# Optimization experiments

Measured on AMD Instinct MI355X. Metric: run time of the kernel, lower is better.

## Reference

```python
import jax, jax.numpy as jnp
import numpy as np

FIELD_DIMS = [100000, 50000, 1000, 500, 100, 50, 20, 10]
INPUT_DIM = sum(FIELD_DIMS)            # 151680
NUM_FIELDS = len(FIELD_DIMS)           # 8
FACTOR_DIM = 16
HIDDEN = [256, 128]
OFFSETS = np.concatenate([[0], np.cumsum(FIELD_DIMS)[:-1]]).astype(np.int32)
BATCH = 2048
EPS = 1e-5


def setup_inputs() -> dict:
    key = jax.random.key(0)
    ks = jax.random.split(key, 32)
    # per-field indices, each within its own cardinality
    x = jnp.stack([
        jax.random.randint(ks[f], (BATCH,), 0, FIELD_DIMS[f], dtype=jnp.int32)
        for f in range(NUM_FIELDS)
    ], axis=1)  # [B, F]
    # concatenated embedding tables (xavier_uniform per torch init, approximated with uniform)
    lim = float(np.sqrt(6.0 / (max(FIELD_DIMS) + FACTOR_DIM)))
    emb_table = jax.random.uniform(ks[8], (INPUT_DIM, FACTOR_DIM), minval=-lim, maxval=lim, dtype=jnp.float32)
    # FM linear: weight ~ N(0, 0.01), bias 0
    w_lin = 0.01 * jax.random.normal(ks[9], (INPUT_DIM,), dtype=jnp.float32)
    b_lin = jnp.zeros((), dtype=jnp.float32)
    d0 = NUM_FIELDS * FACTOR_DIM  # 128
    def lin(k, fan_in, fan_out):
        b = float(np.sqrt(1.0 / fan_in))
        kw, kb = jax.random.split(k)
        W = jax.random.uniform(kw, (fan_in, fan_out), minval=-b, maxval=b, dtype=jnp.float32)
        bias = jax.random.uniform(kb, (fan_out,), minval=-b, maxval=b, dtype=jnp.float32)
        return W, bias
    W1, b1 = lin(ks[10], d0, HIDDEN[0])
    W2, b2 = lin(ks[11], HIDDEN[0], HIDDEN[1])
    W3, b3 = lin(ks[12], HIDDEN[1], 1)
    g1 = jnp.ones((HIDDEN[0],), jnp.float32); be1 = jnp.zeros((HIDDEN[0],), jnp.float32)
    g2 = jnp.ones((HIDDEN[1],), jnp.float32); be2 = jnp.zeros((HIDDEN[1],), jnp.float32)
    return {"x": x, "emb_table": emb_table, "w_lin": w_lin, "b_lin": b_lin,
            "W1": W1, "b1": b1, "g1": g1, "be1": be1,
            "W2": W2, "b2": b2, "g2": g2, "be2": be2,
            "W3": W3, "b3": b3}


def _batchnorm(h, gamma, beta):
    # training-mode BN (torch default): biased batch variance
    m = jnp.mean(h, axis=0)
    v = jnp.mean((h - m) ** 2, axis=0)
    return gamma * (h - m) / jnp.sqrt(v + EPS) + beta


def reference(x, emb_table, w_lin, b_lin, W1, b1, g1, be1, W2, b2, g2, be2, W3, b3):
    B = x.shape[0]
    offsets = jnp.asarray(OFFSETS)
    # --- faithful to original bug: scatter one-hot uses RAW x (no field offsets) ---
    sparse_x = jnp.zeros((B, INPUT_DIM), jnp.float32).at[
        jnp.arange(B)[:, None], x].set(1.0)  # duplicates collapse to 1.0, like scatter_
    y_linear = sparse_x @ w_lin + b_lin  # [B]
    # --- dense field embeddings (offset gather into concatenated table) ---
    dense_x = emb_table[x + offsets[None, :]]  # [B, F, K]
    s = jnp.sum(dense_x, axis=1)               # [B, K]
    square_of_sum = s * s
    sum_of_square = jnp.sum(dense_x * dense_x, axis=1)
    y_pairwise = 0.5 * jnp.sum(square_of_sum - sum_of_square, axis=1)  # [B]
    y_fm = y_linear + y_pairwise
    # --- DNN on concatenated embeddings ---
    h = dense_x.reshape(B, NUM_FIELDS * FACTOR_DIM)
    h = jax.nn.relu(_batchnorm(h @ W1 + b1, g1, be1))
    h = jax.nn.relu(_batchnorm(h @ W2 + b2, g2, be2))
    y_dnn = (h @ W3 + b3)[:, 0]  # [B]
    return y_fm + y_dnn
```

## Files before the change

kernel.cpp:

```cpp
#include <hip/hip_runtime.h>

#define EPS 1e-5f

static __device__ const int OFFS[8] = {0, 100000, 150000, 151000, 151500, 151600, 151650, 151670};

__global__ __launch_bounds__(256) void k1_gather_fm_gemm1(
    const int* __restrict__ x, const float* __restrict__ emb,
    const float* __restrict__ wlin, const float* __restrict__ blin,
    const float* __restrict__ W1, const float* __restrict__ b1,
    float* __restrict__ yfm, float* __restrict__ z1, float* __restrict__ p1)
{
    __shared__ float h0s[16][128];
    const int t = threadIdx.x;
    const int blk = blockIdx.x;
    const int r = t >> 4, l = t & 15;
    const int b = blk * 16 + r;

    int idx[8];
#pragma unroll
    for (int f = 0; f < 8; ++f) idx[f] = x[b * 8 + f];

    float s = 0.f, ssq = 0.f;
#pragma unroll
    for (int f = 0; f < 8; ++f) {
        float e = emb[(idx[f] + OFFS[f]) * 16 + l];
        h0s[r][f * 16 + l] = e;
        s += e;
        ssq += e * e;
    }
    float pair = s * s - ssq;
#pragma unroll
    for (int m = 8; m >= 1; m >>= 1) pair += __shfl_xor(pair, m);

    if (l == 0) {
        float lin = 0.f;
#pragma unroll
        for (int f = 0; f < 8; ++f) {
            bool dup = false;
            for (int g = 0; g < f; ++g) dup = dup || (idx[g] == idx[f]);
            if (!dup) lin += wlin[idx[f]];
        }
        yfm[b] = 0.5f * pair + lin + blin[0];
    }
    __syncthreads();

    const int j = t;
    float acc[16];
#pragma unroll
    for (int r2 = 0; r2 < 16; ++r2) acc[r2] = 0.f;
    for (int k = 0; k < 128; ++k) {
        float w = W1[k * 256 + j];
#pragma unroll
        for (int r2 = 0; r2 < 16; ++r2) acc[r2] += h0s[r2][k] * w;
    }
    const float bj = b1[j];
    float zsum = 0.f, zss = 0.f;
#pragma unroll
    for (int r2 = 0; r2 < 16; ++r2) {
        float z = acc[r2] + bj;
        z1[(blk * 16 + r2) * 256 + j] = z;
        zsum += z;
        zss += z * z;
    }
    p1[blk * 512 + j] = zsum;
    p1[blk * 512 + 256 + j] = zss;
}

__global__ __launch_bounds__(256) void k2_bn1_gemm2(
    const float* __restrict__ z1, const float* __restrict__ p1,
    const float* __restrict__ g1, const float* __restrict__ be1,
    const float* __restrict__ W2, const float* __restrict__ b2,
    float* __restrict__ z2, float* __restrict__ p2)
{
    __shared__ float h1s[32][256];
    __shared__ float psum[2][128];
    __shared__ float pss[2][128];
    const int t = threadIdx.x, blk = blockIdx.x;

    float sum = 0.f, ss = 0.f;
    for (int q = 0; q < 128; ++q) {
        sum += p1[q * 512 + t];
        ss  += p1[q * 512 + 256 + t];
    }
    const float mean = sum * (1.f / 2048.f);
    const float var  = ss * (1.f / 2048.f) - mean * mean;
    const float scale = g1[t] / sqrtf(var + EPS);
    const float shift = be1[t] - mean * scale;

    for (int r = 0; r < 32; ++r) {
        float z = z1[(blk * 32 + r) * 256 + t];
        float h = z * scale + shift;
        h1s[r][t] = h > 0.f ? h : 0.f;
    }
    __syncthreads();

    const int j = t & 127, half = t >> 7;
    float acc[16];
#pragma unroll
    for (int r = 0; r < 16; ++r) acc[r] = 0.f;
    for (int k = 0; k < 256; ++k) {
        float w = W2[k * 128 + j];
#pragma unroll
        for (int r = 0; r < 16; ++r) acc[r] += h1s[half * 16 + r][k] * w;
    }
    const float bj = b2[j];
    float zsum = 0.f, zss = 0.f;
#pragma unroll
    for (int r = 0; r < 16; ++r) {
        float z = acc[r] + bj;
        z2[(blk * 32 + half * 16 + r) * 128 + j] = z;
        zsum += z;
        zss += z * z;
    }
    psum[half][j] = zsum;
    pss[half][j] = zss;
    __syncthreads();
    if (half == 0) {
        p2[blk * 256 + j]       = psum[0][j] + psum[1][j];
        p2[blk * 256 + 128 + j] = pss[0][j] + pss[1][j];
    }
}

__global__ __launch_bounds__(256) void k3_bn2_out(
    const float* __restrict__ z2, const float* __restrict__ p2,
    const float* __restrict__ g2, const float* __restrict__ be2,
    const float* __restrict__ W3, const float* __restrict__ b3,
    const float* __restrict__ yfm, float* __restrict__ out)
{
    __shared__ float scl[128], shf[128];
    const int t = threadIdx.x, blk = blockIdx.x;
    if (t < 128) {
        float sum = 0.f, ss = 0.f;
        for (int q = 0; q < 64; ++q) {
            sum += p2[q * 256 + t];
            ss  += p2[q * 256 + 128 + t];
        }
        const float mean = sum * (1.f / 2048.f);
        const float var  = ss * (1.f / 2048.f) - mean * mean;
        const float sc = g2[t] / sqrtf(var + EPS);
        scl[t] = sc;
        shf[t] = be2[t] - mean * sc;
    }
    __syncthreads();

    const int r = t >> 3, l8 = t & 7;
    const int b = blk * 32 + r;
    float acc = 0.f;
#pragma unroll
    for (int q = 0; q < 16; ++q) {
        int k = q * 8 + l8;
        float z = z2[b * 128 + k];
        float h = z * scl[k] + shf[k];
        h = h > 0.f ? h : 0.f;
        acc += h * W3[k];
    }
#pragma unroll
    for (int m = 4; m >= 1; m >>= 1) acc += __shfl_xor(acc, m);
    if (l8 == 0) out[b] = acc + b3[0] + yfm[b];
}

extern "C" void kernel_launch(void* const* d_in, const int* in_sizes, int n_in,
                              void* d_out, int out_size, void* d_ws, size_t ws_size,
                              hipStream_t stream) {
    const int*   x    = (const int*)d_in[0];
    const float* emb  = (const float*)d_in[1];
    const float* wlin = (const float*)d_in[2];
    const float* blin = (const float*)d_in[3];
    const float* W1   = (const float*)d_in[4];
    const float* b1   = (const float*)d_in[5];
    const float* g1   = (const float*)d_in[6];
    const float* be1  = (const float*)d_in[7];
    const float* W2   = (const float*)d_in[8];
    const float* b2   = (const float*)d_in[9];
    const float* g2   = (const float*)d_in[10];
    const float* be2  = (const float*)d_in[11];
    const float* W3   = (const float*)d_in[12];
    const float* b3   = (const float*)d_in[13];

    float* ws  = (float*)d_ws;
    float* yfm = ws;
    float* z1  = yfm + 2048;
    float* p1  = z1 + 2048 * 256;
    float* z2  = p1 + 128 * 512;
    float* p2  = z2 + 2048 * 128;
    float* out = (float*)d_out;

    k1_gather_fm_gemm1<<<128, 256, 0, stream>>>(x, emb, wlin, blin, W1, b1, yfm, z1, p1);
    k2_bn1_gemm2<<<64, 256, 0, stream>>>(z1, p1, g1, be1, W2, b2, z2, p2);
    k3_bn2_out<<<64, 256, 0, stream>>>(z2, p2, g2, be2, W3, b3, yfm, out);
}
```

Measured before the change: 44.79 us.

## Repartition all three kernels across more blocks with vectorized loads and split reductions

```diff
diff --git a/kernel.cpp b/kernel.cpp
--- a/kernel.cpp
+++ b/kernel.cpp
@@ -10,114 +10,161 @@
     const float* __restrict__ W1, const float* __restrict__ b1,
     float* __restrict__ yfm, float* __restrict__ z1, float* __restrict__ p1)
 {
-    __shared__ float h0s[16][128];
+    __shared__ __align__(16) float h0s[16][128];
+    __shared__ __align__(16) float red[2][8][128];
     const int t = threadIdx.x;
-    const int blk = blockIdx.x;
-    const int r = t >> 4, l = t & 15;
-    const int b = blk * 16 + r;
-
-    int idx[8];
-#pragma unroll
-    for (int f = 0; f < 8; ++f) idx[f] = x[b * 8 + f];
-
-    float s = 0.f, ssq = 0.f;
-#pragma unroll
-    for (int f = 0; f < 8; ++f) {
-        float e = emb[(idx[f] + OFFS[f]) * 16 + l];
-        h0s[r][f * 16 + l] = e;
-        s += e;
-        ssq += e * e;
-    }
-    float pair = s * s - ssq;
-#pragma unroll
-    for (int m = 8; m >= 1; m >>= 1) pair += __shfl_xor(pair, m);
-
-    if (l == 0) {
-        float lin = 0.f;
+    const int rt = blockIdx.x >> 1;
+    const int ch = blockIdx.x & 1;
+
+    {
+        const int g_r = t >> 4, g_l = t & 15;
+        const int b = rt * 16 + g_r;
+        int idx[8];
+#pragma unroll
+        for (int f = 0; f < 8; ++f) idx[f] = x[b * 8 + f];
+
+        float s = 0.f, ssq = 0.f;
 #pragma unroll
         for (int f = 0; f < 8; ++f) {
-            bool dup = false;
-            for (int g = 0; g < f; ++g) dup = dup || (idx[g] == idx[f]);
-            if (!dup) lin += wlin[idx[f]];
-        }
-        yfm[b] = 0.5f * pair + lin + blin[0];
-    }
-    __syncthreads();
-
-    const int j = t;
-    float acc[16];
-#pragma unroll
-    for (int r2 = 0; r2 < 16; ++r2) acc[r2] = 0.f;
-    for (int k = 0; k < 128; ++k) {
-        float w = W1[k * 256 + j];
-#pragma unroll
-        for (int r2 = 0; r2 < 16; ++r2) acc[r2] += h0s[r2][k] * w;
-    }
-    const float bj = b1[j];
-    float zsum = 0.f, zss = 0.f;
-#pragma unroll
-    for (int r2 = 0; r2 < 16; ++r2) {
-        float z = acc[r2] + bj;
-        z1[(blk * 16 + r2) * 256 + j] = z;
-        zsum += z;
-        zss += z * z;
-    }
-    p1[blk * 512 + j] = zsum;
-    p1[blk * 512 + 256 + j] = zss;
-}
-
-__global__ __launch_bounds__(256) void k2_bn1_gemm2(
+            float e = emb[(idx[f] + OFFS[f]) * 16 + g_l];
+            h0s[g_r][f * 16 + g_l] = e;
+            s += e;
+            ssq += e * e;
+        }
+        if (ch == 0) {
+            float pair = s * s - ssq;
+#pragma unroll
+            for (int m = 8; m >= 1; m >>= 1) pair += __shfl_xor(pair, m);
+            if (g_l == 0) {
+                float lin = 0.f;
+#pragma unroll
+                for (int f = 0; f < 8; ++f) {
+                    bool dup = false;
+                    for (int g = 0; g < f; ++g) dup = dup || (idx[g] == idx[f]);
+                    if (!dup) lin += wlin[idx[f]];
+                }
+                yfm[b] = 0.5f * pair + lin + blin[0];
+            }
+        }
+    }
+    __syncthreads();
+
+    const int jg = t & 31, rp = t >> 5;
+    const float* Wb = W1 + ch * 128 + jg * 4;
+    float acc0[4] = {0.f, 0.f, 0.f, 0.f};
+    float acc1[4] = {0.f, 0.f, 0.f, 0.f};
+    for (int k = 0; k < 128; k += 4) {
+        float4 ha = *(const float4*)&h0s[rp * 2][k];
+        float4 hb = *(const float4*)&h0s[rp * 2 + 1][k];
+        const float ha_[4] = {ha.x, ha.y, ha.z, ha.w};
+        const float hb_[4] = {hb.x, hb.y, hb.z, hb.w};
+#pragma unroll
+        for (int kk = 0; kk < 4; ++kk) {
+            float4 w = *(const float4*)&Wb[(k + kk) * 256];
+            acc0[0] += ha_[kk] * w.x; acc0[1] += ha_[kk] * w.y;
+            acc0[2] += ha_[kk] * w.z; acc0[3] += ha_[kk] * w.w;
+            acc1[0] += hb_[kk] * w.x; acc1[1] += hb_[kk] * w.y;
+            acc1[2] += hb_[kk] * w.z; acc1[3] += hb_[kk] * w.w;
+        }
+    }
+    float4 bj = *(const float4*)&b1[ch * 128 + jg * 4];
+    const float bj_[4] = {bj.x, bj.y, bj.z, bj.w};
+    float zs[4], zss[4];
+    float z0[4], z1v[4];
+#pragma unroll
+    for (int c = 0; c < 4; ++c) {
+        z0[c] = acc0[c] + bj_[c];
+        z1v[c] = acc1[c] + bj_[c];
+        zs[c] = z0[c] + z1v[c];
+        zss[c] = z0[c] * z0[c] + z1v[c] * z1v[c];
+    }
+    const int r0 = rt * 16 + rp * 2;
+    *(float4*)&z1[r0 * 256 + ch * 128 + jg * 4] = make_float4(z0[0], z0[1], z0[2], z0[3]);
+    *(float4*)&z1[(r0 + 1) * 256 + ch * 128 + jg * 4] = make_float4(z1v[0], z1v[1], z1v[2], z1v[3]);
+    *(float4*)&red[0][rp][jg * 4] = make_float4(zs[0], zs[1], zs[2], zs[3]);
+    *(float4*)&red[1][rp][jg * 4] = make_float4(zss[0], zss[1], zss[2], zss[3]);
+    __syncthreads();
+    if (t < 128) {
+        float s = 0.f, ss = 0.f;
+#pragma unroll
+        for (int q = 0; q < 8; ++q) { s += red[0][q][t]; ss += red[1][q][t]; }
+        p1[rt * 512 + ch * 128 + t] = s;
+        p1[rt * 512 + 256 + ch * 128 + t] = ss;
+    }
+}
+
+__global__ __launch_bounds__(512) void k2_bn1_gemm2(
     const float* __restrict__ z1, const float* __restrict__ p1,
     const float* __restrict__ g1, const float* __restrict__ be1,
     const float* __restrict__ W2, const float* __restrict__ b2,
     float* __restrict__ z2, float* __restrict__ p2)
 {
-    __shared__ float h1s[32][256];
-    __shared__ float psum[2][128];
-    __shared__ float pss[2][128];
-    const int t = threadIdx.x, blk = blockIdx.x;
-
-    float sum = 0.f, ss = 0.f;
-    for (int q = 0; q < 128; ++q) {
-        sum += p1[q * 512 + t];
-        ss  += p1[q * 512 + 256 + t];
-    }
-    const float mean = sum * (1.f / 2048.f);
-    const float var  = ss * (1.f / 2048.f) - mean * mean;
-    const float scale = g1[t] / sqrtf(var + EPS);
-    const float shift = be1[t] - mean * scale;
-
-    for (int r = 0; r < 32; ++r) {
-        float z = z1[(blk * 32 + r) * 256 + t];
-        float h = z * scale + shift;
-        h1s[r][t] = h > 0.f ? h : 0.f;
-    }
-    __syncthreads();
-
-    const int j = t & 127, half = t >> 7;
-    float acc[16];
-#pragma unroll
-    for (int r = 0; r < 16; ++r) acc[r] = 0.f;
-    for (int k = 0; k < 256; ++k) {
-        float w = W2[k * 128 + j];
-#pragma unroll
-        for (int r = 0; r < 16; ++r) acc[r] += h1s[half * 16 + r][k] * w;
-    }
-    const float bj = b2[j];
-    float zsum = 0.f, zss = 0.f;
-#pragma unroll
-    for (int r = 0; r < 16; ++r) {
-        float z = acc[r] + bj;
-        z2[(blk * 32 + half * 16 + r) * 128 + j] = z;
-        zsum += z;
-        zss += z * z;
-    }
-    psum[half][j] = zsum;
-    pss[half][j] = zss;
-    __syncthreads();
-    if (half == 0) {
-        p2[blk * 256 + j]       = psum[0][j] + psum[1][j];
-        p2[blk * 256 + 128 + j] = pss[0][j] + pss[1][j];
+    __shared__ __align__(16) float h1s[8][256];
+    __shared__ __align__(16) float sclS[256], shfS[256];
+    __shared__ __align__(16) float sp[2][256], ssp[2][256];
+    __shared__ __align__(16) float red2[2][8][128];
+    const int t = threadIdx.x, rb = blockIdx.x;
+
+    {
+        const int col = t & 255, h = t >> 8;
+        float s = 0.f, ss = 0.f;
+#pragma unroll 16
+        for (int q = h * 64; q < h * 64 + 64; ++q) {
+            s += p1[q * 512 + col];
+            ss += p1[q * 512 + 256 + col];
+        }
+        sp[h][col] = s; ssp[h][col] = ss;
+    }
+    __syncthreads();
+    if (t < 256) {
+        float s = sp[0][t] + sp[1][t];
+        float ss = ssp[0][t] + ssp[1][t];
+        float mean = s * (1.f / 2048.f);
+        float var = ss * (1.f / 2048.f) - mean * mean;
+        float sc = g1[t] * __frsqrt_rn(var + EPS);
+        sclS[t] = sc;
+        shfS[t] = be1[t] - mean * sc;
+    }
+    __syncthreads();
+
+    {
+        const int lr = t >> 6, lc = (t & 63) * 4;
+        float4 zv = *(const float4*)&z1[(rb * 8 + lr) * 256 + lc];
+        float4 sc = *(const float4*)&sclS[lc];
+        float4 sh = *(const float4*)&shfS[lc];
+        float4 hv;
+        hv.x = fmaxf(zv.x * sc.x + sh.x, 0.f);
+        hv.y = fmaxf(zv.y * sc.y + sh.y, 0.f);
+        hv.z = fmaxf(zv.z * sc.z + sh.z, 0.f);
+        hv.w = fmaxf(zv.w * sc.w + sh.w, 0.f);
+        *(float4*)&h1s[lr][lc] = hv;
+    }
+    __syncthreads();
+
+    const int r = t >> 6, j2 = (t & 63) * 2;
+    float acc[2] = {0.f, 0.f};
+    for (int k = 0; k < 256; k += 4) {
+        float4 hv = *(const float4*)&h1s[r][k];
+        const float h_[4] = {hv.x, hv.y, hv.z, hv.w};
+#pragma unroll
+        for (int kk = 0; kk < 4; ++kk) {
+            float2 w = *(const float2*)&W2[(k + kk) * 128 + j2];
+            acc[0] += h_[kk] * w.x;
+            acc[1] += h_[kk] * w.y;
+        }
+    }
+    float2 bj = *(const float2*)&b2[j2];
+    float za = acc[0] + bj.x, zb = acc[1] + bj.y;
+    *(float2*)&z2[(rb * 8 + r) * 128 + j2] = make_float2(za, zb);
+    *(float2*)&red2[0][r][j2] = make_float2(za, zb);
+    *(float2*)&red2[1][r][j2] = make_float2(za * za, zb * zb);
+    __syncthreads();
+    if (t < 128) {
+        float s = 0.f, ss = 0.f;
+#pragma unroll
+        for (int q = 0; q < 8; ++q) { s += red2[0][q][t]; ss += red2[1][q][t]; }
+        p2[rb * 256 + t] = s;
+        p2[rb * 256 + 128 + t] = ss;
     }
 }
 
@@ -127,36 +174,44 @@
     const float* __restrict__ W3, const float* __restrict__ b3,
     const float* __restrict__ yfm, float* __restrict__ out)
 {
-    __shared__ float scl[128], shf[128];
+    __shared__ __align__(16) float sp[2][128], ssp[2][128];
+    __shared__ __align__(16) float scl[128], shf[128];
     const int t = threadIdx.x, blk = blockIdx.x;
+    {
+        const int col = t & 127, h = t >> 7;
+        float s = 0.f, ss = 0.f;
+#pragma unroll 16
+        for (int q = h * 128; q < h * 128 + 128; ++q) {
+            s += p2[q * 256 + col];
+            ss += p2[q * 256 + 128 + col];
+        }
+        sp[h][col] = s; ssp[h][col] = ss;
+    }
+    __syncthreads();
     if (t < 128) {
-        float sum = 0.f, ss = 0.f;
-        for (int q = 0; q < 64; ++q) {
-            sum += p2[q * 256 + t];
-            ss  += p2[q * 256 + 128 + t];
-        }
-        const float mean = sum * (1.f / 2048.f);
-        const float var  = ss * (1.f / 2048.f) - mean * mean;
-        const float sc = g2[t] / sqrtf(var + EPS);
+        float s = sp[0][t] + sp[1][t];
+        float ss = ssp[0][t] + ssp[1][t];
+        float mean = s * (1.f / 2048.f);
+        float var = ss * (1.f / 2048.f) - mean * mean;
+        float sc = g2[t] * __frsqrt_rn(var + EPS);
         scl[t] = sc;
         shf[t] = be2[t] - mean * sc;
     }
     __syncthreads();
 
-    const int r = t >> 3, l8 = t & 7;
-    const int b = blk * 32 + r;
-    float acc = 0.f;
-#pragma unroll
-    for (int q = 0; q < 16; ++q) {
-        int k = q * 8 + l8;
-        float z = z2[b * 128 + k];
-        float h = z * scl[k] + shf[k];
-        h = h > 0.f ? h : 0.f;
-        acc += h * W3[k];
-    }
-#pragma unroll
-    for (int m = 4; m >= 1; m >>= 1) acc += __shfl_xor(acc, m);
-    if (l8 == 0) out[b] = acc + b3[0] + yfm[b];
+    const int r = t >> 5, l32 = t & 31;
+    const int b = blk * 8 + r;
+    float4 zv = *(const float4*)&z2[b * 128 + l32 * 4];
+    float4 sc = *(const float4*)&scl[l32 * 4];
+    float4 sh = *(const float4*)&shf[l32 * 4];
+    float4 wv = *(const float4*)&W3[l32 * 4];
+    float acc = fmaxf(zv.x * sc.x + sh.x, 0.f) * wv.x
+              + fmaxf(zv.y * sc.y + sh.y, 0.f) * wv.y
+              + fmaxf(zv.z * sc.z + sh.z, 0.f) * wv.z
+              + fmaxf(zv.w * sc.w + sh.w, 0.f) * wv.w;
+#pragma unroll
+    for (int m = 16; m >= 1; m >>= 1) acc += __shfl_xor(acc, m);
+    if (l32 == 0) out[b] = acc + b3[0] + yfm[b];
 }
 
 extern "C" void kernel_launch(void* const* d_in, const int* in_sizes, int n_in,
@@ -185,7 +240,7 @@
     float* p2  = z2 + 2048 * 128;
     float* out = (float*)d_out;
 
-    k1_gather_fm_gemm1<<<128, 256, 0, stream>>>(x, emb, wlin, blin, W1, b1, yfm, z1, p1);
-    k2_bn1_gemm2<<<64, 256, 0, stream>>>(z1, p1, g1, be1, W2, b2, z2, p2);
-    k3_bn2_out<<<64, 256, 0, stream>>>(z2, p2, g2, be2, W3, b3, yfm, out);
-}
+    k1_gather_fm_gemm1<<<256, 256, 0, stream>>>(x, emb, wlin, blin, W1, b1, yfm, z1, p1);
+    k2_bn1_gemm2<<<256, 512, 0, stream>>>(z1, p1, g1, be1, W2, b2, z2, p2);
+    k3_bn2_out<<<256, 256, 0, stream>>>(z2, p2, g2, be2, W3, b3, yfm, out);
+}
```

Result: faster. 37.84 us (-15.5%).

## Fuse three DeepFM kernels into one cooperative kernel with grid syncs

Applied to the files above, without the earlier changes.

```diff
diff --git a/kernel.cpp b/kernel.cpp
--- a/kernel.cpp
+++ b/kernel.cpp
@@ -1,162 +1,236 @@
 #include <hip/hip_runtime.h>
+#include <hip/hip_cooperative_groups.h>
+
+namespace cg = cooperative_groups;
 
 #define EPS 1e-5f
 
 static __device__ const int OFFS[8] = {0, 100000, 150000, 151000, 151500, 151600, 151650, 151670};
 
-__global__ __launch_bounds__(256) void k1_gather_fm_gemm1(
+__global__ __launch_bounds__(256) void deepfm_fused(
     const int* __restrict__ x, const float* __restrict__ emb,
     const float* __restrict__ wlin, const float* __restrict__ blin,
     const float* __restrict__ W1, const float* __restrict__ b1,
-    float* __restrict__ yfm, float* __restrict__ z1, float* __restrict__ p1)
-{
-    __shared__ float h0s[16][128];
-    const int t = threadIdx.x;
-    const int blk = blockIdx.x;
-    const int r = t >> 4, l = t & 15;
-    const int b = blk * 16 + r;
-
-    int idx[8];
-#pragma unroll
-    for (int f = 0; f < 8; ++f) idx[f] = x[b * 8 + f];
-
-    float s = 0.f, ssq = 0.f;
-#pragma unroll
-    for (int f = 0; f < 8; ++f) {
-        float e = emb[(idx[f] + OFFS[f]) * 16 + l];
-        h0s[r][f * 16 + l] = e;
-        s += e;
-        ssq += e * e;
-    }
-    float pair = s * s - ssq;
-#pragma unroll
-    for (int m = 8; m >= 1; m >>= 1) pair += __shfl_xor(pair, m);
-
-    if (l == 0) {
-        float lin = 0.f;
-#pragma unroll
-        for (int f = 0; f < 8; ++f) {
-            bool dup = false;
-            for (int g = 0; g < f; ++g) dup = dup || (idx[g] == idx[f]);
-            if (!dup) lin += wlin[idx[f]];
-        }
-        yfm[b] = 0.5f * pair + lin + blin[0];
-    }
-    __syncthreads();
-
-    const int j = t;
-    float acc[16];
-#pragma unroll
-    for (int r2 = 0; r2 < 16; ++r2) acc[r2] = 0.f;
-    for (int k = 0; k < 128; ++k) {
-        float w = W1[k * 256 + j];
-#pragma unroll
-        for (int r2 = 0; r2 < 16; ++r2) acc[r2] += h0s[r2][k] * w;
-    }
-    const float bj = b1[j];
-    float zsum = 0.f, zss = 0.f;
-#pragma unroll
-    for (int r2 = 0; r2 < 16; ++r2) {
-        float z = acc[r2] + bj;
-        z1[(blk * 16 + r2) * 256 + j] = z;
-        zsum += z;
-        zss += z * z;
-    }
-    p1[blk * 512 + j] = zsum;
-    p1[blk * 512 + 256 + j] = zss;
-}
-
-__global__ __launch_bounds__(256) void k2_bn1_gemm2(
-    const float* __restrict__ z1, const float* __restrict__ p1,
     const float* __restrict__ g1, const float* __restrict__ be1,
     const float* __restrict__ W2, const float* __restrict__ b2,
-    float* __restrict__ z2, float* __restrict__ p2)
-{
-    __shared__ float h1s[32][256];
-    __shared__ float psum[2][128];
-    __shared__ float pss[2][128];
-    const int t = threadIdx.x, blk = blockIdx.x;
-
-    float sum = 0.f, ss = 0.f;
-    for (int q = 0; q < 128; ++q) {
-        sum += p1[q * 512 + t];
-        ss  += p1[q * 512 + 256 + t];
-    }
-    const float mean = sum * (1.f / 2048.f);
-    const float var  = ss * (1.f / 2048.f) - mean * mean;
-    const float scale = g1[t] / sqrtf(var + EPS);
-    const float shift = be1[t] - mean * scale;
-
-    for (int r = 0; r < 32; ++r) {
-        float z = z1[(blk * 32 + r) * 256 + t];
-        float h = z * scale + shift;
-        h1s[r][t] = h > 0.f ? h : 0.f;
-    }
-    __syncthreads();
-
-    const int j = t & 127, half = t >> 7;
-    float acc[16];
-#pragma unroll
-    for (int r = 0; r < 16; ++r) acc[r] = 0.f;
-    for (int k = 0; k < 256; ++k) {
-        float w = W2[k * 128 + j];
-#pragma unroll
-        for (int r = 0; r < 16; ++r) acc[r] += h1s[half * 16 + r][k] * w;
-    }
-    const float bj = b2[j];
-    float zsum = 0.f, zss = 0.f;
-#pragma unroll
-    for (int r = 0; r < 16; ++r) {
-        float z = acc[r] + bj;
-        z2[(blk * 32 + half * 16 + r) * 128 + j] = z;
-        zsum += z;
-        zss += z * z;
-    }
-    psum[half][j] = zsum;
-    pss[half][j] = zss;
-    __syncthreads();
-    if (half == 0) {
-        p2[blk * 256 + j]       = psum[0][j] + psum[1][j];
-        p2[blk * 256 + 128 + j] = pss[0][j] + pss[1][j];
-    }
-}
-
-__global__ __launch_bounds__(256) void k3_bn2_out(
-    const float* __restrict__ z2, const float* __restrict__ p2,
     const float* __restrict__ g2, const float* __restrict__ be2,
     const float* __restrict__ W3, const float* __restrict__ b3,
-    const float* __restrict__ yfm, float* __restrict__ out)
+    float* __restrict__ p1g, float* __restrict__ s1g,
+    float* __restrict__ p2g, float* __restrict__ s2g,
+    float* __restrict__ out)
 {
-    __shared__ float scl[128], shf[128];
+    cg::grid_group grid = cg::this_grid();
+
+    __shared__ __align__(16) float h0s[8][128];
+    __shared__ __align__(16) float h1s[8][256];
+    __shared__ __align__(16) float redA[8][256];
+    __shared__ __align__(16) float redB[8][256];
+    __shared__ __align__(16) float wsS[4][4], wsQ[4][4];
+    __shared__ float yfmS[8];
+
     const int t = threadIdx.x, blk = blockIdx.x;
+    const int rp = t >> 5, l = t & 31;
+    const int row = blk * 8 + rp;
+
+    {
+        const int f = l >> 2, dq = (l & 3) * 4;
+        const int idxf = x[row * 8 + f];
+        float4 e = *(const float4*)&emb[(size_t)(idxf + OFFS[f]) * 16 + dq];
+        *(float4*)&h0s[rp][f * 16 + dq] = e;
+
+        float4 s = e;
+        float4 q = make_float4(e.x * e.x, e.y * e.y, e.z * e.z, e.w * e.w);
+#pragma unroll
+        for (int m = 4; m <= 16; m <<= 1) {
+            s.x += __shfl_xor(s.x, m); s.y += __shfl_xor(s.y, m);
+            s.z += __shfl_xor(s.z, m); s.w += __shfl_xor(s.w, m);
+            q.x += __shfl_xor(q.x, m); q.y += __shfl_xor(q.y, m);
+            q.z += __shfl_xor(q.z, m); q.w += __shfl_xor(q.w, m);
+        }
+        float pair = (s.x * s.x - q.x) + (s.y * s.y - q.y)
+                   + (s.z * s.z - q.z) + (s.w * s.w - q.w);
+        pair += __shfl_xor(pair, 1);
+        pair += __shfl_xor(pair, 2);
+
+        float lin = 0.f;
+        if (l < 8) {
+            int ids[8];
+#pragma unroll
+            for (int f2 = 0; f2 < 8; ++f2) ids[f2] = x[row * 8 + f2];
+            bool dup = false;
+            for (int g = 0; g < l; ++g) dup = dup || (ids[g] == ids[l]);
+            lin = dup ? 0.f : wlin[ids[l]];
+        }
+        lin += __shfl_xor(lin, 1);
+        lin += __shfl_xor(lin, 2);
+        lin += __shfl_xor(lin, 4);
+        if (l == 0) yfmS[rp] = 0.5f * pair + lin + blin[0];
+    }
+    __syncthreads();
+
+    float z1r[8];
+    {
+        float acc[8] = {0.f, 0.f, 0.f, 0.f, 0.f, 0.f, 0.f, 0.f};
+        const float* Wb = W1 + l * 8;
+        for (int k = 0; k < 128; k += 4) {
+            float4 h4 = *(const float4*)&h0s[rp][k];
+            const float h_[4] = {h4.x, h4.y, h4.z, h4.w};
+#pragma unroll
+            for (int kk = 0; kk < 4; ++kk) {
+                float4 wA = *(const float4*)&Wb[(k + kk) * 256];
+                float4 wB = *(const float4*)&Wb[(k + kk) * 256 + 4];
+                acc[0] += h_[kk] * wA.x; acc[1] += h_[kk] * wA.y;
+                acc[2] += h_[kk] * wA.z; acc[3] += h_[kk] * wA.w;
+                acc[4] += h_[kk] * wB.x; acc[5] += h_[kk] * wB.y;
+                acc[6] += h_[kk] * wB.z; acc[7] += h_[kk] * wB.w;
+            }
+        }
+        float4 bA = *(const float4*)&b1[l * 8];
+        float4 bB = *(const float4*)&b1[l * 8 + 4];
+        z1r[0] = acc[0] + bA.x; z1r[1] = acc[1] + bA.y;
+        z1r[2] = acc[2] + bA.z; z1r[3] = acc[3] + bA.w;
+        z1r[4] = acc[4] + bB.x; z1r[5] = acc[5] + bB.y;
+        z1r[6] = acc[6] + bB.z; z1r[7] = acc[7] + bB.w;
+
+        *(float4*)&redA[rp][l * 8]     = make_float4(z1r[0], z1r[1], z1r[2], z1r[3]);
+        *(float4*)&redA[rp][l * 8 + 4] = make_float4(z1r[4], z1r[5], z1r[6], z1r[7]);
+        *(float4*)&redB[rp][l * 8]     = make_float4(z1r[0]*z1r[0], z1r[1]*z1r[1], z1r[2]*z1r[2], z1r[3]*z1r[3]);
+        *(float4*)&redB[rp][l * 8 + 4] = make_float4(z1r[4]*z1r[4], z1r[5]*z1r[5], z1r[6]*z1r[6], z1r[7]*z1r[7]);
+    }
+    __syncthreads();
+    {
+        float s = 0.f, q = 0.f;
+#pragma unroll
+        for (int r = 0; r < 8; ++r) { s += redA[r][t]; q += redB[r][t]; }
+        p1g[blk * 512 + t] = s;
+        p1g[blk * 512 + 256 + t] = q;
+    }
+
+    grid.sync();
+
+    if (blk < 64) {
+        float4 sA = *(const float4*)&p1g[t * 512 + blk * 4];
+        float4 sB = *(const float4*)&p1g[t * 512 + 256 + blk * 4];
+#pragma unroll
+        for (int m = 1; m <= 32; m <<= 1) {
+            sA.x += __shfl_xor(sA.x, m); sA.y += __shfl_xor(sA.y, m);
+            sA.z += __shfl_xor(sA.z, m); sA.w += __shfl_xor(sA.w, m);
+            sB.x += __shfl_xor(sB.x, m); sB.y += __shfl_xor(sB.y, m);
+            sB.z += __shfl_xor(sB.z, m); sB.w += __shfl_xor(sB.w, m);
+        }
+        if ((t & 63) == 0) {
+            const int w = t >> 6;
+            *(float4*)&wsS[w][0] = sA;
+            *(float4*)&wsQ[w][0] = sB;
+        }
+        __syncthreads();
+        if (t < 4) {
+            const int c = blk * 4 + t;
+            float s = wsS[0][t] + wsS[1][t] + wsS[2][t] + wsS[3][t];
+            float q = wsQ[0][t] + wsQ[1][t] + wsQ[2][t] + wsQ[3][t];
+            float mean = s * (1.f / 2048.f);
+            float var  = q * (1.f / 2048.f) - mean * mean;
+            float sc = g1[c] * __frsqrt_rn(var + EPS);
+            s1g[c] = sc;
+            s1g[256 + c] = be1[c] - mean * sc;
+        }
+    }
+
+    grid.sync();
+
+    {
+        float4 scA = *(const float4*)&s1g[l * 8];
+        float4 scB = *(const float4*)&s1g[l * 8 + 4];
+        float4 shA = *(const float4*)&s1g[256 + l * 8];
+        float4 shB = *(const float4*)&s1g[256 + l * 8 + 4];
+        float4 hA, hB;
+        hA.x = fmaxf(z1r[0] * scA.x + shA.x, 0.f);
+        hA.y = fmaxf(z1r[1] * scA.y + shA.y, 0.f);
+        hA.z = fmaxf(z1r[2] * scA.z + shA.z, 0.f);
+        hA.w = fmaxf(z1r[3] * scA.w + shA.w, 0.f);
+        hB.x = fmaxf(z1r[4] * scB.x + shB.x, 0.f);
+        hB.y = fmaxf(z1r[5] * scB.y + shB.y, 0.f);
+        hB.z = fmaxf(z1r[6] * scB.z + shB.z, 0.f);
+        hB.w = fmaxf(z1r[7] * scB.w + shB.w, 0.f);
+        *(float4*)&h1s[rp][l * 8] = hA;
+        *(float4*)&h1s[rp][l * 8 + 4] = hB;
+    }
+    __syncthreads();
+
+    float z2r[4];
+    {
+        float acc[4] = {0.f, 0.f, 0.f, 0.f};
+        const float* Wb = W2 + l * 4;
+        for (int k = 0; k < 256; k += 4) {
+            float4 h4 = *(const float4*)&h1s[rp][k];
+            const float h_[4] = {h4.x, h4.y, h4.z, h4.w};
+#pragma unroll
+            for (int kk = 0; kk < 4; ++kk) {
+                float4 w = *(const float4*)&Wb[(k + kk) * 128];
+                acc[0] += h_[kk] * w.x; acc[1] += h_[kk] * w.y;
+                acc[2] += h_[kk] * w.z; acc[3] += h_[kk] * w.w;
+            }
+        }
+        float4 b4 = *(const float4*)&b2[l * 4];
+        z2r[0] = acc[0] + b4.x; z2r[1] = acc[1] + b4.y;
+        z2r[2] = acc[2] + b4.z; z2r[3] = acc[3] + b4.w;
+    }
+    __syncthreads();
+    *(float4*)&redA[rp][l * 4] = make_float4(z2r[0], z2r[1], z2r[2], z2r[3]);
+    *(float4*)&redB[rp][l * 4] = make_float4(z2r[0]*z2r[0], z2r[1]*z2r[1], z2r[2]*z2r[2], z2r[3]*z2r[3]);
+    __syncthreads();
     if (t < 128) {
-        float sum = 0.f, ss = 0.f;
-        for (int q = 0; q < 64; ++q) {
-            sum += p2[q * 256 + t];
-            ss  += p2[q * 256 + 128 + t];
-        }
-        const float mean = sum * (1.f / 2048.f);
-        const float var  = ss * (1.f / 2048.f) - mean * mean;
-        const float sc = g2[t] / sqrtf(var + EPS);
-        scl[t] = sc;
-        shf[t] = be2[t] - mean * sc;
-    }
-    __syncthreads();
-
-    const int r = t >> 3, l8 = t & 7;
-    const int b = blk * 32 + r;
-    float acc = 0.f;
-#pragma unroll
-    for (int q = 0; q < 16; ++q) {
-        int k = q * 8 + l8;
-        float z = z2[b * 128 + k];
-        float h = z * scl[k] + shf[k];
-        h = h > 0.f ? h : 0.f;
-        acc += h * W3[k];
-    }
-#pragma unroll
-    for (int m = 4; m >= 1; m >>= 1) acc += __shfl_xor(acc, m);
-    if (l8 == 0) out[b] = acc + b3[0] + yfm[b];
+        float s = 0.f, q = 0.f;
+#pragma unroll
+        for (int r = 0; r < 8; ++r) { s += redA[r][t]; q += redB[r][t]; }
+        p2g[blk * 256 + t] = s;
+        p2g[blk * 256 + 128 + t] = q;
+    }
+
+    grid.sync();
+
+    if (blk < 32) {
+        float4 sA = *(const float4*)&p2g[t * 256 + blk * 4];
+        float4 sB = *(const float4*)&p2g[t * 256 + 128 + blk * 4];
+#pragma unroll
+        for (int m = 1; m <= 32; m <<= 1) {
+            sA.x += __shfl_xor(sA.x, m); sA.y += __shfl_xor(sA.y, m);
+            sA.z += __shfl_xor(sA.z, m); sA.w += __shfl_xor(sA.w, m);
+            sB.x += __shfl_xor(sB.x, m); sB.y += __shfl_xor(sB.y, m);
+            sB.z += __shfl_xor(sB.z, m); sB.w += __shfl_xor(sB.w, m);
+        }
+        if ((t & 63) == 0) {
+            const int w = t >> 6;
+            *(float4*)&wsS[w][0] = sA;
+            *(float4*)&wsQ[w][0] = sB;
+        }
+        __syncthreads();
+        if (t < 4) {
+            const int c = blk * 4 + t;
+            float s = wsS[0][t] + wsS[1][t] + wsS[2][t] + wsS[3][t];
+            float q = wsQ[0][t] + wsQ[1][t] + wsQ[2][t] + wsQ[3][t];
+            float mean = s * (1.f / 2048.f);
+            float var  = q * (1.f / 2048.f) - mean * mean;
+            float sc = g2[c] * __frsqrt_rn(var + EPS);
+            s2g[c] = sc;
+            s2g[128 + c] = be2[c] - mean * sc;
+        }
+    }
+
+    grid.sync();
+
+    {
+        float4 sc = *(const float4*)&s2g[l * 4];
+        float4 sh = *(const float4*)&s2g[128 + l * 4];
+        float4 w3 = *(const float4*)&W3[l * 4];
+        float acc = fmaxf(z2r[0] * sc.x + sh.x, 0.f) * w3.x
+                  + fmaxf(z2r[1] * sc.y + sh.y, 0.f) * w3.y
+                  + fmaxf(z2r[2] * sc.z + sh.z, 0.f) * w3.z
+                  + fmaxf(z2r[3] * sc.w + sh.w, 0.f) * w3.w;
+#pragma unroll
+        for (int m = 16; m >= 1; m >>= 1) acc += __shfl_xor(acc, m);
+        if (l == 0) out[row] = acc + b3[0] + yfmS[rp];
+    }
 }
 
 extern "C" void kernel_launch(void* const* d_in, const int* in_sizes, int n_in,
@@ -178,14 +252,19 @@
     const float* b3   = (const float*)d_in[13];
 
     float* ws  = (float*)d_ws;
-    float* yfm = ws;
-    float* z1  = yfm + 2048;
-    float* p1  = z1 + 2048 * 256;
-    float* z2  = p1 + 128 * 512;
-    float* p2  = z2 + 2048 * 128;
+    float* p1g = ws;
+    float* s1g = p1g + 256 * 512;
+    float* p2g = s1g + 512;
+    float* s2g = p2g + 256 * 256;
     float* out = (float*)d_out;
 
-    k1_gather_fm_gemm1<<<128, 256, 0, stream>>>(x, emb, wlin, blin, W1, b1, yfm, z1, p1);
-    k2_bn1_gemm2<<<64, 256, 0, stream>>>(z1, p1, g1, be1, W2, b2, z2, p2);
-    k3_bn2_out<<<64, 256, 0, stream>>>(z2, p2, g2, be2, W3, b3, yfm, out);
+    void* args[] = {
+        (void*)&x, (void*)&emb, (void*)&wlin, (void*)&blin,
+        (void*)&W1, (void*)&b1, (void*)&g1, (void*)&be1,
+        (void*)&W2, (void*)&b2, (void*)&g2, (void*)&be2,
+        (void*)&W3, (void*)&b3,
+        (void*)&p1g, (void*)&s1g, (void*)&p2g, (void*)&s2g, (void*)&out
+    };
+    hipLaunchCooperativeKernel((void*)deepfm_fused, dim3(256), dim3(256),
+                               args, 0, stream);
 }
```

Measured after the change: 154.5 us. +244.9%, slower.
